# Kernel tuning notes

Hardware: AMD Instinct MI355X
Metric: run time of the kernel (lower is better)

The kernel has to match this reference:

```python
import jax, jax.numpy as jnp
import numpy as np

EMB = 1024
HEADS = 16
SCALE = (EMB // HEADS) ** (-0.5)


def setup_inputs() -> dict:
    key = jax.random.key(0)
    k1, k2, k3, k4, k5 = jax.random.split(key, 5)
    x = jax.random.normal(k1, (2, 2048, EMB), dtype=jnp.float32)
    w_qkv = jax.random.normal(k2, (EMB, 3 * EMB), dtype=jnp.float32) * (EMB ** -0.5)
    b_qkv = jax.random.normal(k3, (3 * EMB,), dtype=jnp.float32) * 0.02
    w_proj = jax.random.normal(k4, (EMB, EMB), dtype=jnp.float32) * (EMB ** -0.5)
    b_proj = jax.random.normal(k5, (EMB,), dtype=jnp.float32) * 0.02
    return {"x": x, "w_qkv": w_qkv, "b_qkv": b_qkv, "w_proj": w_proj, "b_proj": b_proj}


def reference(x, w_qkv, b_qkv, w_proj, b_proj):
    b, n, d = x.shape
    # qkv projection; split last dim as (heads, head_dim, 3) exactly like the
    # torch reshape, then permute to (3, b, h, n, head_dim)
    qkv = (x @ w_qkv + b_qkv).reshape(b, n, HEADS, -1, 3)
    qkv = jnp.transpose(qkv, (4, 0, 2, 1, 3))
    q, k, v = qkv[0], qkv[1], qkv[2]
    energy = jnp.einsum('bhqd,bhkd->bhqk', q, k)  # full n x n scores
    att = jax.nn.softmax(energy, axis=-1) * SCALE  # softmax THEN scale (as in source)
    out = jnp.einsum('bhqk,bhkd->bhqd', att, v)
    out = jnp.transpose(out, (0, 2, 1, 3)).reshape(b, n, d)
    return out @ w_proj + b_proj
```

## Files before the change

kernel.cpp:

```cpp
#include <hip/hip_runtime.h>
#include <cstdint>

#define SEQ   2048
#define BATCH 2
#define EMB   1024
#define NH    16
#define HD    64
#define MROWS (BATCH*SEQ)
#define NQKV  (3*EMB)
#define SCALE 0.125f
#define L2E   1.4426950408889634f

typedef _Float16 half8 __attribute__((ext_vector_type(8)));
typedef _Float16 half4 __attribute__((ext_vector_type(4)));
typedef __fp16   fp16x2 __attribute__((ext_vector_type(2)));
typedef float    floatx4 __attribute__((ext_vector_type(4)));

#define MFMA(a,b,c) __builtin_amdgcn_mfma_f32_16x16x32_f16(a, b, c, 0, 0, 0)

__device__ __forceinline__ void async16(const void* g, const void* l) {
    __builtin_amdgcn_global_load_lds(
        (const __attribute__((address_space(1))) unsigned int*)(uintptr_t)g,
        (__attribute__((address_space(3))) unsigned int*)(uint32_t)(uintptr_t)l,
        16, 0, 0);
}

__global__ void k_split(const float* __restrict__ src, _Float16* __restrict__ hi, int n4) {
    int i = blockIdx.x * blockDim.x + threadIdx.x;
    if (i >= n4) return;
    float4 v = ((const float4*)src)[i];
    half4 h;
    h[0] = (_Float16)v.x;
    h[1] = (_Float16)v.y;
    h[2] = (_Float16)v.z;
    h[3] = (_Float16)v.w;
    ((half4*)hi)[i] = h;
}

__global__ void k_transpose_split(const float* __restrict__ w, _Float16* __restrict__ hi,
                                  int K, int N) {
    __shared__ float t[32][33];
    int n0 = blockIdx.x * 32, k0 = blockIdx.y * 32;
    int tx = threadIdx.x, ty = threadIdx.y;
    #pragma unroll
    for (int i = 0; i < 4; i++)
        t[ty + i * 8][tx] = w[(size_t)(k0 + ty + i * 8) * N + n0 + tx];
    __syncthreads();
    #pragma unroll
    for (int i = 0; i < 4; i++) {
        float v = t[tx][ty + i * 8];
        hi[(size_t)(n0 + ty + i * 8) * K + k0 + tx] = (_Float16)v;
    }
}

template<int MODE, int NT>
__global__ __launch_bounds__(256, 2)
void k_gemm(const _Float16* __restrict__ A, const _Float16* __restrict__ Bt,
            const float* __restrict__ bias,
            _Float16* __restrict__ outQ, _Float16* __restrict__ outK,
            _Float16* __restrict__ outV, float* __restrict__ outC,
            int Mdim, int Ndim, int Kdim) {
    constexpr int WN  = NT / 2;
    constexpr int NTI = WN / 16;
    __shared__ _Float16 smem[(128 + NT) * 32];
    _Float16* As = smem;
    _Float16* Bs = smem + 128 * 32;

    const int tid = threadIdx.x;
    const int lane = tid & 63, wid = tid >> 6;
    const int quad = lane >> 4, l16 = lane & 15;
    const int wm = (wid >> 1) * 64, wn = (wid & 1) * WN;
    const int m0 = blockIdx.y * 128, n0 = blockIdx.x * NT;

    floatx4 acc[4][NTI];
    #pragma unroll
    for (int i = 0; i < 4; i++)
        #pragma unroll
        for (int j = 0; j < NTI; j++)
            acc[i][j] = (floatx4){0.f, 0.f, 0.f, 0.f};

    for (int k0 = 0; k0 < Kdim; k0 += 32) {
        __syncthreads();
        #pragma unroll
        for (int i = 0; i < 2; i++) {
            int c = i * 256 + tid;
            int row = c >> 2, slot = c & 3;
            int q = slot ^ ((row >> 1) & 3);
            async16(A + (size_t)(m0 + row) * Kdim + k0 + q * 8, As + c * 8);
        }
        #pragma unroll
        for (int i = 0; i < NT / 64; i++) {
            int c = i * 256 + tid;
            int row = c >> 2, slot = c & 3;
            int q = slot ^ ((row >> 1) & 3);
            async16(Bt + (size_t)(n0 + row) * Kdim + k0 + q * 8, Bs + c * 8);
        }
        __syncthreads();

        half8 af[4], bf[NTI];
        #pragma unroll
        for (int t = 0; t < 4; t++) {
            int rowA = wm + t * 16 + l16;
            af[t] = *(const half8*)(As + rowA * 32 + (quad ^ ((rowA >> 1) & 3)) * 8);
        }
        #pragma unroll
        for (int t = 0; t < NTI; t++) {
            int rowB = wn + t * 16 + l16;
            bf[t] = *(const half8*)(Bs + rowB * 32 + (quad ^ ((rowB >> 1) & 3)) * 8);
        }
        #pragma unroll
        for (int mt = 0; mt < 4; mt++)
            #pragma unroll
            for (int nt = 0; nt < NTI; nt++)
                acc[mt][nt] = MFMA(af[mt], bf[nt], acc[mt][nt]);
    }

    #pragma unroll
    for (int mt = 0; mt < 4; mt++) {
        int rowg = m0 + wm + mt * 16 + quad * 4;
        #pragma unroll
        for (int nt = 0; nt < NTI; nt++) {
            int colg = n0 + wn + nt * 16 + l16;
            float bv = bias[colg];
            if (MODE == 0) {
                int h = colg / 192, rem = colg % 192;
                int d = rem / 3, which = rem % 3;
                #pragma unroll
                for (int r = 0; r < 4; r++) {
                    int m = rowg + r;
                    int b = m >> 11, s = m & (SEQ - 1);
                    int bh = b * NH + h;
                    _Float16 hv = (_Float16)(acc[mt][nt][r] + bv);
                    if (which == 0)      outQ[((size_t)bh * SEQ + s) * HD + d] = hv;
                    else if (which == 1) outK[((size_t)bh * SEQ + s) * HD + d] = hv;
                    else                 outV[((size_t)bh * HD + d) * SEQ + s] = hv;
                }
            } else {
                #pragma unroll
                for (int r = 0; r < 4; r++)
                    outC[(size_t)(rowg + r) * Ndim + colg] = acc[mt][nt][r] + bv;
            }
        }
    }
}

__device__ __forceinline__ int swzK(int row) { return (row ^ (row >> 2)) & 7; }
__device__ __forceinline__ int swzV(int row) { return (row ^ (row >> 1)) & 7; }

__global__ __launch_bounds__(256, 2)
void k_attn(const _Float16* __restrict__ Q, const _Float16* __restrict__ K,
            const _Float16* __restrict__ Vt, _Float16* __restrict__ Aout) {
    __shared__ __align__(16) _Float16 Ks[2][128 * 64];
    __shared__ __align__(16) _Float16 Vs[2][80 * 128];

    const int tid = threadIdx.x;
    const int lane = tid & 63, wid = tid >> 6;
    const int quad = lane >> 4, l16 = lane & 15;

    const int n = blockIdx.x;
    const int bh = (n & 7) * 4 + (n >> 7);
    const int q0 = ((n >> 3) & 15) * 128;

    const _Float16* Qb = Q  + (size_t)bh * SEQ * HD;
    const _Float16* Kb = K  + (size_t)bh * SEQ * HD;
    const _Float16* Vb = Vt + (size_t)bh * HD * SEQ;

    const int rA = ((l16 >> 2) << 3) | (l16 & 3);
    const int grayl = (l16 ^ (l16 >> 1)) & 7;

    {
        half8 one8;
        #pragma unroll
        for (int r = 0; r < 8; r++) one8[r] = (_Float16)1.0f;
        ((half8*)(Vs[0] + 64 * 128))[tid] = one8;
        ((half8*)(Vs[1] + 64 * 128))[tid] = one8;
    }
    __syncthreads();

    half8 qf[2][2];
    #pragma unroll
    for (int qt = 0; qt < 2; qt++)
        #pragma unroll
        for (int kc = 0; kc < 2; kc++)
            qf[qt][kc] = *(const half8*)(Qb + (size_t)(q0 + wid * 32 + qt * 16 + l16) * HD
                                          + kc * 32 + quad * 8);

    #pragma unroll
    for (int i = 0; i < 4; i++) {
        int c = i * 256 + tid;
        int rowK = c >> 3, posK = c & 7;
        async16(Kb + (size_t)rowK * HD + (posK ^ swzK(rowK)) * 8, Ks[0] + c * 8);
        int rowV = c >> 4, posV = c & 15;
        int qv = (posV & 8) | ((posV & 7) ^ swzV(rowV));
        async16(Vb + (size_t)rowV * SEQ + qv * 8, Vs[0] + c * 8);
    }

    floatx4 o[2][4], o_l[2];
    float mi[2] = {-1e30f, -1e30f};
    #pragma unroll
    for (int qt = 0; qt < 2; qt++) {
        #pragma unroll
        for (int dt = 0; dt < 4; dt++) o[qt][dt] = (floatx4){0.f, 0.f, 0.f, 0.f};
        o_l[qt] = (floatx4){0.f, 0.f, 0.f, 0.f};
    }

    #pragma unroll 2
    for (int t = 0; t < 16; t++) {
        const int p = t & 1;
        const int kvn = ((t + 1) & 15) * 128;
        #pragma unroll
        for (int i = 0; i < 4; i++) {
            int c = i * 256 + tid;
            int rowK = c >> 3, posK = c & 7;
            async16(Kb + (size_t)(kvn + rowK) * HD + (posK ^ swzK(rowK)) * 8,
                    Ks[p ^ 1] + c * 8);
            int rowV = c >> 4, posV = c & 15;
            int qv = (posV & 8) | ((posV & 7) ^ swzV(rowV));
            async16(Vb + (size_t)rowV * SEQ + kvn + qv * 8, Vs[p ^ 1] + c * 8);
        }
        asm volatile("s_waitcnt vmcnt(8)" ::: "memory");
        asm volatile("s_barrier" ::: "memory");

        const _Float16* Ksp = Ks[p];
        const _Float16* Vsp = Vs[p];

        floatx4 sv[4][2][2];
        #pragma unroll
        for (int u = 0; u < 4; u++)
            #pragma unroll
            for (int e = 0; e < 2; e++) {
                int row = u * 32 + e * 4 + rA;
                int sw = swzK(row);
                const _Float16* base = Ksp + row * 64;
                half8 kf0 = *(const half8*)(base + ((quad ^ sw) << 3));
                half8 kf1 = *(const half8*)(base + (((quad + 4) ^ sw) << 3));
                floatx4 z = (floatx4){0.f, 0.f, 0.f, 0.f};
                #pragma unroll
                for (int qt = 0; qt < 2; qt++) {
                    floatx4 s = MFMA(kf0, qf[qt][0], z);
                    sv[u][e][qt] = MFMA(kf1, qf[qt][1], s);
                }
            }

        #pragma unroll
        for (int qt = 0; qt < 2; qt++) {
            float mb = -1e30f;
            #pragma unroll
            for (int u = 0; u < 4; u++)
                #pragma unroll
                for (int e = 0; e < 2; e++)
                    #pragma unroll
                    for (int r = 0; r < 4; r++)
                        mb = fmaxf(mb, sv[u][e][qt][r]);
            mb = fmaxf(mb, __shfl_xor(mb, 16));
            mb = fmaxf(mb, __shfl_xor(mb, 32));
            float Mn = fmaxf(mi[qt], mb * L2E);
            float al = __builtin_amdgcn_exp2f(mi[qt] - Mn);
            mi[qt] = Mn;
            float alq[4];
            #pragma unroll
            for (int r = 0; r < 4; r++)
                alq[r] = __shfl(al, quad * 4 + r);
            #pragma unroll
            for (int dt = 0; dt < 4; dt++)
                #pragma unroll
                for (int r = 0; r < 4; r++)
                    o[qt][dt][r] *= alq[r];
            #pragma unroll
            for (int r = 0; r < 4; r++)
                o_l[qt][r] *= alq[r];
        }

        #pragma unroll
        for (int u = 0; u < 4; u++) {
            half8 af[2];
            #pragma unroll
            for (int qt = 0; qt < 2; qt++) {
                float p0[8];
                #pragma unroll
                for (int r = 0; r < 4; r++) {
                    p0[r]     = __builtin_amdgcn_exp2f(fmaf(sv[u][0][qt][r], L2E, -mi[qt]));
                    p0[4 + r] = __builtin_amdgcn_exp2f(fmaf(sv[u][1][qt][r], L2E, -mi[qt]));
                }
                union { fp16x2 h2[4]; half8 v; } pk;
                pk.h2[0] = __builtin_amdgcn_cvt_pkrtz(p0[0], p0[1]);
                pk.h2[1] = __builtin_amdgcn_cvt_pkrtz(p0[2], p0[3]);
                pk.h2[2] = __builtin_amdgcn_cvt_pkrtz(p0[4], p0[5]);
                pk.h2[3] = __builtin_amdgcn_cvt_pkrtz(p0[6], p0[7]);
                af[qt] = pk.v;
            }
            int q = u * 4 + quad;
            int slotbase = (q & 8) | ((q & 7) ^ grayl);
            #pragma unroll
            for (int dt = 0; dt < 4; dt++) {
                int row = dt * 16 + l16;
                half8 vf = *(const half8*)(Vsp + row * 128 + slotbase * 8);
                o[0][dt] = MFMA(af[0], vf, o[0][dt]);
                o[1][dt] = MFMA(af[1], vf, o[1][dt]);
            }
            half8 vfl = *(const half8*)(Vsp + (64 + l16) * 128 + slotbase * 8);
            o_l[0] = MFMA(af[0], vfl, o_l[0]);
            o_l[1] = MFMA(af[1], vfl, o_l[1]);
        }

        asm volatile("s_barrier" ::: "memory");
    }

    int b = bh >> 4, h = bh & 15;
    #pragma unroll
    for (int qt = 0; qt < 2; qt++)
        #pragma unroll
        for (int r = 0; r < 4; r++) {
            float inv = SCALE / o_l[qt][r];
            int srow = q0 + wid * 32 + qt * 16 + quad * 4 + r;
            #pragma unroll
            for (int dt = 0; dt < 4; dt++) {
                int col = h * HD + dt * 16 + l16;
                Aout[(size_t)(b * SEQ + srow) * EMB + col] = (_Float16)(o[qt][dt][r] * inv);
            }
        }
}

extern "C" void kernel_launch(void* const* d_in, const int* in_sizes, int n_in,
                              void* d_out, int out_size, void* d_ws, size_t ws_size,
                              hipStream_t stream) {
    (void)in_sizes; (void)n_in; (void)out_size; (void)ws_size;
    const float* x      = (const float*)d_in[0];
    const float* w_qkv  = (const float*)d_in[1];
    const float* b_qkv  = (const float*)d_in[2];
    const float* w_proj = (const float*)d_in[3];
    const float* b_proj = (const float*)d_in[4];

    char* ws = (char*)d_ws;
    const size_t MB = 1ull << 20;
    _Float16* x_hi  = (_Float16*)(ws + 0 * MB);
    _Float16* wq_hi = (_Float16*)(ws + 8 * MB);
    _Float16* wp_hi = (_Float16*)(ws + 14 * MB);
    _Float16* Qb    = (_Float16*)(ws + 16 * MB);
    _Float16* Kb    = (_Float16*)(ws + 24 * MB);
    _Float16* Vtb   = (_Float16*)(ws + 32 * MB);
    _Float16* attb  = (_Float16*)(ws + 40 * MB);

    k_split<<<(MROWS * EMB / 4) / 256, 256, 0, stream>>>(x, x_hi, MROWS * EMB / 4);
    k_transpose_split<<<dim3(NQKV / 32, EMB / 32), dim3(32, 8), 0, stream>>>(
        w_qkv, wq_hi, EMB, NQKV);
    k_transpose_split<<<dim3(EMB / 32, EMB / 32), dim3(32, 8), 0, stream>>>(
        w_proj, wp_hi, EMB, EMB);
    k_gemm<0, 128><<<dim3(NQKV / 128, MROWS / 128), 256, 0, stream>>>(
        x_hi, wq_hi, b_qkv, Qb, Kb, Vtb, nullptr, MROWS, NQKV, EMB);
    k_attn<<<dim3(512), 256, 0, stream>>>(Qb, Kb, Vtb, attb);
    k_gemm<1, 64><<<dim3(EMB / 64, MROWS / 128), 256, 0, stream>>>(
        attb, wp_hi, b_proj, nullptr, nullptr, nullptr,
        (float*)d_out, MROWS, EMB, EMB);
}
```

Measured before the change: 197.7 us.

## Double-buffer GEMM shared-memory tiles with async prefetch of next K slice

The GEMM main loop now uses two LDS buffers: the next K tile is issued via async global-to-LDS loads before computing on the current tile. A partial vmcnt wait and raw s_barriers replace the full syncthreads pair, so global load latency can overlap with MFMA work. LDS use doubles, which may lower occupancy, and the last iteration issues a redundant prefetch of tile 0. The hand-written waitcnt values assume an exact count of outstanding loads.

```diff
diff --git a/kernel.cpp b/kernel.cpp
--- a/kernel.cpp
+++ b/kernel.cpp
@@ -62,9 +62,8 @@
             int Mdim, int Ndim, int Kdim) {
     constexpr int WN  = NT / 2;
     constexpr int NTI = WN / 16;
-    __shared__ _Float16 smem[(128 + NT) * 32];
-    _Float16* As = smem;
-    _Float16* Bs = smem + 128 * 32;
+    constexpr int LB  = NT / 64;
+    __shared__ _Float16 smem[2][(128 + NT) * 32];
 
     const int tid = threadIdx.x;
     const int lane = tid & 63, wid = tid >> 6;
@@ -72,6 +71,27 @@
     const int wm = (wid >> 1) * 64, wn = (wid & 1) * WN;
     const int m0 = blockIdx.y * 128, n0 = blockIdx.x * NT;
 
+    const int row4 = tid >> 2, slot4 = tid & 3;
+
+    auto stage = [&](int k0, int buf) {
+        _Float16* As = smem[buf];
+        _Float16* Bs = smem[buf] + 128 * 32;
+        #pragma unroll
+        for (int i = 0; i < 2; i++) {
+            int c = i * 256 + tid;
+            int row = i * 64 + row4;
+            int q = slot4 ^ ((row >> 1) & 3);
+            async16(A + (size_t)(m0 + row) * Kdim + k0 + q * 8, As + c * 8);
+        }
+        #pragma unroll
+        for (int i = 0; i < LB; i++) {
+            int c = i * 256 + tid;
+            int row = i * 64 + row4;
+            int q = slot4 ^ ((row >> 1) & 3);
+            async16(Bt + (size_t)(n0 + row) * Kdim + k0 + q * 8, Bs + c * 8);
+        }
+    };
+
     floatx4 acc[4][NTI];
     #pragma unroll
     for (int i = 0; i < 4; i++)
@@ -79,24 +99,19 @@
         for (int j = 0; j < NTI; j++)
             acc[i][j] = (floatx4){0.f, 0.f, 0.f, 0.f};
 
-    for (int k0 = 0; k0 < Kdim; k0 += 32) {
-        __syncthreads();
-        #pragma unroll
-        for (int i = 0; i < 2; i++) {
-            int c = i * 256 + tid;
-            int row = c >> 2, slot = c & 3;
-            int q = slot ^ ((row >> 1) & 3);
-            async16(A + (size_t)(m0 + row) * Kdim + k0 + q * 8, As + c * 8);
-        }
-        #pragma unroll
-        for (int i = 0; i < NT / 64; i++) {
-            int c = i * 256 + tid;
-            int row = c >> 2, slot = c & 3;
-            int q = slot ^ ((row >> 1) & 3);
-            async16(Bt + (size_t)(n0 + row) * Kdim + k0 + q * 8, Bs + c * 8);
-        }
-        __syncthreads();
-
+    const int NIT = Kdim >> 5;
+    stage(0, 0);
+
+    for (int it = 0; it < NIT; it++) {
+        const int p = it & 1;
+        const int k0n = ((it + 1 == NIT) ? 0 : (it + 1)) << 5;
+        stage(k0n, p ^ 1);
+        if constexpr (LB == 2) asm volatile("s_waitcnt vmcnt(4)" ::: "memory");
+        else                   asm volatile("s_waitcnt vmcnt(3)" ::: "memory");
+        asm volatile("s_barrier" ::: "memory");
+
+        const _Float16* As = smem[p];
+        const _Float16* Bs = smem[p] + 128 * 32;
         half8 af[4], bf[NTI];
         #pragma unroll
         for (int t = 0; t < 4; t++) {
@@ -113,6 +128,8 @@
             #pragma unroll
             for (int nt = 0; nt < NTI; nt++)
                 acc[mt][nt] = MFMA(af[mt], bf[nt], acc[mt][nt]);
+
+        asm volatile("s_barrier" ::: "memory");
     }
 
     #pragma unroll
```

Result: slower. 201.9 us (+2.1%).
